# Kernel tuning notes

Measured on AMD Instinct MI355X. Metric: run time of the kernel, lower is better.

Reference implementation:

```python
import jax, jax.numpy as jnp
import numpy as np

N_NODES = 20000
N_EDGES = 160000
N_GRAPHS = 1000
IN_DIM = 11
HID = 128
EDGE_DIM = 3
N_LAYERS = 5
BN_EPS = 1e-5


def setup_inputs() -> dict:
    key = jax.random.key(0)
    ks = jax.random.split(key, 24)
    x = jax.random.normal(ks[0], (N_NODES, IN_DIM), dtype=jnp.float32)
    edge_index = jax.random.randint(ks[1], (2, N_EDGES), 0, N_NODES, dtype=jnp.int64)
    batch = jnp.sort(jax.random.randint(ks[2], (N_NODES,), 0, N_GRAPHS, dtype=jnp.int64))
    edge_attr = jax.random.uniform(ks[3], (N_EDGES, EDGE_DIM), dtype=jnp.float32)
    s_in = 1.0 / np.sqrt(IN_DIM)
    s_z = 1.0 / np.sqrt(2 * HID + EDGE_DIM)
    s_h = 1.0 / np.sqrt(HID)
    W_in = jax.random.uniform(ks[4], (IN_DIM, HID), minval=-s_in, maxval=s_in)
    b_in = jax.random.uniform(ks[5], (HID,), minval=-s_in, maxval=s_in)
    Wf = jax.random.uniform(ks[6], (N_LAYERS, 2 * HID + EDGE_DIM, HID), minval=-s_z, maxval=s_z)
    bf = jax.random.uniform(ks[7], (N_LAYERS, HID), minval=-s_z, maxval=s_z)
    Ws = jax.random.uniform(ks[8], (N_LAYERS, 2 * HID + EDGE_DIM, HID), minval=-s_z, maxval=s_z)
    bs = jax.random.uniform(ks[9], (N_LAYERS, HID), minval=-s_z, maxval=s_z)
    gamma = jnp.ones((N_LAYERS, HID), dtype=jnp.float32)
    beta = jnp.zeros((N_LAYERS, HID), dtype=jnp.float32)
    W1 = jax.random.uniform(ks[10], (HID, HID), minval=-s_h, maxval=s_h)
    b1 = jax.random.uniform(ks[11], (HID,), minval=-s_h, maxval=s_h)
    W2 = jax.random.uniform(ks[12], (HID, HID), minval=-s_h, maxval=s_h)
    b2 = jax.random.uniform(ks[13], (HID,), minval=-s_h, maxval=s_h)
    W3 = jax.random.uniform(ks[14], (HID, 1), minval=-s_h, maxval=s_h)
    b3 = jax.random.uniform(ks[15], (1,), minval=-s_h, maxval=s_h)
    return {"x": x, "edge_index": edge_index, "batch": batch, "edge_attr": edge_attr,
            "W_in": W_in, "b_in": b_in, "Wf": Wf, "bf": bf, "Ws": Ws, "bs": bs,
            "gamma": gamma, "beta": beta, "W1": W1, "b1": b1, "W2": W2, "b2": b2,
            "W3": W3, "b3": b3}


def reference(x, edge_index, batch, edge_attr, W_in, b_in, Wf, bf, Ws, bs,
              gamma, beta, W1, b1, W2, b2, W3, b3):
    src = edge_index[0]  # x_j (source / neighbor)
    dst = edge_index[1]  # x_i (target / aggregation index)
    # in-degree per node for mean aggregation (zero-degree -> divide by 1, yields 0)
    deg = jax.ops.segment_sum(jnp.ones((N_EDGES,), jnp.float32), dst, num_segments=N_NODES)
    deg = jnp.maximum(deg, 1.0)[:, None]

    h = x @ W_in + b_in  # [N, H]
    for l in range(N_LAYERS):
        # CGConv: z = [x_i, x_j, e]; msg = sigmoid(z Wf) * softplus(z Ws); residual + mean-aggr
        z = jnp.concatenate([h[dst], h[src], edge_attr], axis=-1)  # [E, 2H+D]
        msg = jax.nn.sigmoid(z @ Wf[l] + bf[l]) * jax.nn.softplus(z @ Ws[l] + bs[l])
        agg = jax.ops.segment_sum(msg, dst, num_segments=N_NODES) / deg
        h = h + agg
        # BatchNorm1d (training-mode batch stats, biased variance)
        mu = jnp.mean(h, axis=0)
        var = jnp.mean((h - mu) ** 2, axis=0)
        h = (h - mu) * jax.lax.rsqrt(var + BN_EPS) * gamma[l] + beta[l]
        h = jax.nn.relu(h)
        # dropout omitted (eval mode)

    # global mean pool over graphs
    cnt = jax.ops.segment_sum(jnp.ones((N_NODES,), jnp.float32), batch, num_segments=N_GRAPHS)
    g = jax.ops.segment_sum(h, batch, num_segments=N_GRAPHS) / jnp.maximum(cnt, 1.0)[:, None]

    g = jax.nn.relu(g @ W1 + b1)
    g = jax.nn.relu(g @ W2 + b2)
    return g @ W3 + b3  # [G, 1]
```

## Files before the change

### kernel.cpp

```cpp
#include <hip/hip_runtime.h>
#include <math.h>

#define NN 20000
#define NE 160000
#define NG 1000
#define IND 11
#define H 128
#define ED 3
#define NL 5
#define ZDH (259*128)
#define BN_EPSF 1e-5f
#define BPAD 17
#define EPW 16
#define GP 4

#define DEG_BLKS ((NE + 255) / 256)
#define WPREP_BLKS ((NL * 512 * H + 255) / 256)
#define GB_BLKS ((NN + 255) / 256)
#define HIN_BLKS 512
#define PREP_GRID (DEG_BLKS + WPREP_BLKS + GB_BLKS + HIN_BLKS)

typedef unsigned short ushort_t;
typedef unsigned int uint_t;
typedef __attribute__((ext_vector_type(8))) short bf8_t;
typedef __attribute__((ext_vector_type(4))) float f4_t;

__device__ inline ushort_t f2bf(float x) {
    unsigned int u = __float_as_uint(x);
    unsigned int r = (u + 0x7fffu + ((u >> 16) & 1u)) >> 16;
    return (ushort_t)r;
}
__device__ inline float bf2f(ushort_t b) {
    return __uint_as_float(((unsigned int)b) << 16);
}

__global__ __launch_bounds__(256) void prep_fused(const int* __restrict__ dst,
                                                  int* __restrict__ degi,
                                                  const float* __restrict__ Wf,
                                                  const float* __restrict__ Ws,
                                                  ushort_t* __restrict__ Wt,
                                                  const float* __restrict__ x,
                                                  const float* __restrict__ Win,
                                                  const float* __restrict__ bin,
                                                  float* __restrict__ h,
                                                  const int* __restrict__ batch,
                                                  int* __restrict__ gstart) {
    int b = blockIdx.x;
    int tid = threadIdx.x;
    if (b < DEG_BLKS) {
        int e = b * 256 + tid;
        if (e < NE) atomicAdd(&degi[dst[e]], 1);
    } else if (b < DEG_BLKS + WPREP_BLKS) {
        int idx = (b - DEG_BLKS) * 256 + tid;
        if (idx < NL * 512 * H) {
            int k = idx & 127;
            int n = (idx >> 7) & 511;
            int l = idx >> 16;
            int t = n >> 7, j = n & 127;
            const float* W = (t == 0 || t == 2) ? Wf : Ws;
            int krow = (t < 2) ? k : (H + k);
            Wt[idx] = f2bf(W[(size_t)l * ZDH + krow * H + j]);
        }
    } else if (b < DEG_BLKS + WPREP_BLKS + GB_BLKS) {
        int n = (b - DEG_BLKS - WPREP_BLKS) * 256 + tid;
        if (n < NN) {
            int b0 = batch[n];
            int bn = (n + 1 < NN) ? batch[n + 1] : NG;
            if (n == 0)
                for (int t = 0; t <= b0; ++t) gstart[t] = 0;
            for (int t = b0 + 1; t <= bn; ++t) gstart[t] = n + 1;
        }
    } else {
        __shared__ float lw[IND * H];
        for (int i = tid; i < IND * H; i += 256) lw[i] = Win[i];
        __syncthreads();
        int j = tid & 127;
        float bj = bin[j];
        int rb = b - (DEG_BLKS + WPREP_BLKS + GB_BLKS);
        for (int n = rb * 2 + (tid >> 7); n < NN; n += HIN_BLKS * 2) {
            const float* xr = x + (size_t)n * IND;
            float acc = bj;
#pragma unroll
            for (int k = 0; k < IND; ++k) acc = fmaf(xr[k], lw[k * H + j], acc);
            h[(size_t)n * H + j] = acc;
        }
    }
}

__global__ __launch_bounds__(256) void reserve_kernel(const int* __restrict__ degi,
                                                      int* __restrict__ cursor,
                                                      float* __restrict__ invdeg,
                                                      int* __restrict__ counter) {
    int n = blockIdx.x * blockDim.x + threadIdx.x;
    int lane = threadIdx.x & 63;
    int v = (n < NN) ? degi[n] : 0;
    int x = v;
#pragma unroll
    for (int st = 1; st < 64; st <<= 1) {
        int y = __shfl_up(x, st, 64);
        if (lane >= st) x += y;
    }
    int total = __shfl(x, 63, 64);
    int base = 0;
    if (lane == 63) base = atomicAdd(counter, total);
    base = __shfl(base, 63, 64);
    if (n < NN) {
        cursor[n] = base + x - v;
        invdeg[n] = 1.0f / (float)(v < 1 ? 1 : v);
    }
}

__global__ void scatter_kernel(const int* __restrict__ src, const int* __restrict__ dst,
                               const float* __restrict__ ea,
                               const float* __restrict__ invdeg,
                               int* __restrict__ cursor, float4* __restrict__ csr_ea4,
                               int* __restrict__ csr_dst, float* __restrict__ csr_inv) {
    int e = blockIdx.x * blockDim.x + threadIdx.x;
    if (e < NE) {
        int d = dst[e];
        int pos = atomicAdd(&cursor[d], 1);
        float4 r;
        r.x = ea[e * ED + 0];
        r.y = ea[e * ED + 1];
        r.z = ea[e * ED + 2];
        r.w = __int_as_float(src[e]);
        csr_ea4[pos] = r;
        csr_dst[pos] = d;
        csr_inv[pos] = invdeg[d];
    }
}

__global__ void flag_kernel(const int* __restrict__ csr_dst, unsigned* __restrict__ endmask) {
    int e = blockIdx.x * blockDim.x + threadIdx.x;
    if (e < NE) {
        int d = csr_dst[e];
        int dn = (e + 1 < NE) ? csr_dst[e + 1] : -1;
        if (d != dn) atomicOr(&endmask[e >> 5], 1u << (e & 31));
    }
}

__global__ __launch_bounds__(256, 2) void node_gemm_mfma(const float* __restrict__ hsrc,
                                                         float* __restrict__ hbn,
                                                         const ushort_t* __restrict__ Wt,
                                                         const float* __restrict__ sum,
                                                         const float* __restrict__ sumsq,
                                                         const float* __restrict__ gamma,
                                                         const float* __restrict__ beta,
                                                         int applyBN,
                                                         uint_t* __restrict__ ppack,
                                                         uint_t* __restrict__ qpack) {
    __shared__ __align__(16) ushort_t lbF[128 * BPAD * 8];
    __shared__ __align__(16) ushort_t lbS[128 * BPAD * 8];
    int pair = blockIdx.y;
    int wave = threadIdx.x >> 6;
    int lane = threadIdx.x & 63;
    int sub = lane & 15;
    int quad = lane >> 4;
    int m0 = blockIdx.x * 64 + wave * 16;
    int writeH = applyBN && (pair == 0);

    const ushort_t* whF = Wt + (size_t)(2 * pair) * 128 * H;
    const ushort_t* whS = Wt + (size_t)(2 * pair + 1) * 128 * H;

    for (int c = threadIdx.x; c < 2048; c += 256) {
        int n = c >> 4, k = c & 15;
        *(bf8_t*)(lbF + ((size_t)n * BPAD + k) * 8) = *(const bf8_t*)(whF + n * H + k * 8);
        *(bf8_t*)(lbS + ((size_t)n * BPAD + k) * 8) = *(const bf8_t*)(whS + n * H + k * 8);
    }

    bf8_t aHi[4], aLo[4];
    int r = m0 + sub;
    int rc = r < NN ? r : NN - 1;
#pragma unroll
    for (int ks = 0; ks < 4; ++ks) {
        int kb = ks * 32 + quad * 8;
        const float* hp = hsrc + (size_t)rc * H + kb;
        float4 v0 = *(const float4*)hp;
        float4 v1 = *(const float4*)(hp + 4);
        float vv[8] = {v0.x, v0.y, v0.z, v0.w, v1.x, v1.y, v1.z, v1.w};
        if (applyBN) {
            float4 su0 = *(const float4*)&sum[kb],   su1 = *(const float4*)&sum[kb + 4];
            float4 sq0 = *(const float4*)&sumsq[kb], sq1 = *(const float4*)&sumsq[kb + 4];
            float4 ga0 = *(const float4*)&gamma[kb], ga1 = *(const float4*)&gamma[kb + 4];
            float4 be0 = *(const float4*)&beta[kb],  be1 = *(const float4*)&beta[kb + 4];
            float su[8] = {su0.x, su0.y, su0.z, su0.w, su1.x, su1.y, su1.z, su1.w};
            float sq[8] = {sq0.x, sq0.y, sq0.z, sq0.w, sq1.x, sq1.y, sq1.z, sq1.w};
            float ga[8] = {ga0.x, ga0.y, ga0.z, ga0.w, ga1.x, ga1.y, ga1.z, ga1.w};
            float be[8] = {be0.x, be0.y, be0.z, be0.w, be1.x, be1.y, be1.z, be1.w};
#pragma unroll
            for (int i = 0; i < 8; ++i) {
                float mu  = su[i] * (1.0f / NN);
                float var = sq[i] * (1.0f / NN) - mu * mu;
                float sc  = ga[i] * rsqrtf(var + BN_EPSF);
                float sh  = be[i] - mu * sc;
                float v = fmaf(vv[i], sc, sh);
                vv[i] = v > 0.0f ? v : 0.0f;
            }
        }
        bf8_t hi8, lo8;
#pragma unroll
        for (int i = 0; i < 8; ++i) {
            ushort_t hi = f2bf(vv[i]);
            hi8[i] = (short)hi;
            lo8[i] = (short)f2bf(vv[i] - bf2f(hi));
        }
        aHi[ks] = hi8;
        aLo[ks] = lo8;
        if (writeH && r < NN) {
            float* op = hbn + (size_t)r * H + kb;
            *(float4*)op = make_float4(vv[0], vv[1], vv[2], vv[3]);
            *(float4*)(op + 4) = make_float4(vv[4], vv[5], vv[6], vv[7]);
        }
    }
    __syncthreads();

    f4_t accF[8], accS[8];
#pragma unroll
    for (int b = 0; b < 8; ++b) { accF[b] = (f4_t){0.f, 0.f, 0.f, 0.f}; accS[b] = (f4_t){0.f, 0.f, 0.f, 0.f}; }

#pragma unroll
    for (int nt = 0; nt < 8; ++nt) {
#pragma unroll
        for (int ks = 0; ks < 4; ++ks) {
            size_t lo = ((size_t)(nt * 16 + sub) * BPAD + ks * 4 + quad) * 8;
            bf8_t bF = *(const bf8_t*)(lbF + lo);
            bf8_t bS = *(const bf8_t*)(lbS + lo);
            accF[nt] = __builtin_amdgcn_mfma_f32_16x16x32_bf16(aHi[ks], bF, accF[nt], 0, 0, 0);
            accF[nt] = __builtin_amdgcn_mfma_f32_16x16x32_bf16(aLo[ks], bF, accF[nt], 0, 0, 0);
            accS[nt] = __builtin_amdgcn_mfma_f32_16x16x32_bf16(aHi[ks], bS, accS[nt], 0, 0, 0);
            accS[nt] = __builtin_amdgcn_mfma_f32_16x16x32_bf16(aLo[ks], bS, accS[nt], 0, 0, 0);
        }
    }

    uint_t* outp = pair ? qpack : ppack;
#pragma unroll
    for (int nt = 0; nt < 8; ++nt) {
        int col = nt * 16 + sub;
#pragma unroll
        for (int rr = 0; rr < 4; ++rr) {
            int row = m0 + quad * 4 + rr;
            if (row < NN) {
                uint_t lo = f2bf(accF[nt][rr]);
                uint_t hi = f2bf(accS[nt][rr]);
                outp[(size_t)row * H + col] = lo | (hi << 16);
            }
        }
    }
}

__global__ __launch_bounds__(256) void agg_edge_kernel(const int4* __restrict__ csr_fe,
                                                       const int* __restrict__ csr_dst,
                                                       const float* __restrict__ csr_inv,
                                                       const unsigned* __restrict__ endmask,
                                                       const float* __restrict__ Wf,
                                                       const float* __restrict__ bf,
                                                       const float* __restrict__ Ws,
                                                       const float* __restrict__ bs,
                                                       const uint_t* __restrict__ ppack,
                                                       const uint_t* __restrict__ qpack,
                                                       float* __restrict__ h,
                                                       float* __restrict__ sum,
                                                       float* __restrict__ sumsq) {
    int tid = threadIdx.x;
    if (blockIdx.x == 0 && tid < H) { sum[tid] = 0.0f; sumsq[tid] = 0.0f; }
    int lane = tid & 63;
    int wv = tid >> 6;
    int base = (blockIdx.x * 4 + wv) * EPW;
    int c0 = 2 * lane;

    float2 wf0 = *(const float2*)&Wf[256 * H + c0];
    float2 wf1 = *(const float2*)&Wf[257 * H + c0];
    float2 wf2 = *(const float2*)&Wf[258 * H + c0];
    float2 ws0 = *(const float2*)&Ws[256 * H + c0];
    float2 ws1 = *(const float2*)&Ws[257 * H + c0];
    float2 ws2 = *(const float2*)&Ws[258 * H + c0];
    float2 bf2_ = *(const float2*)&bf[c0];
    float2 bs2_ = *(const float2*)&bs[c0];

    int4 fe = csr_fe[base + (lane & (EPW - 1))];
    int  dd = csr_dst[base + (lane & (EPW - 1))];
    int  ivr = __float_as_int(csr_inv[base + (lane & (EPW - 1))]);
    unsigned mword = endmask[base >> 5];
    unsigned mask = __builtin_amdgcn_readfirstlane((mword >> (base & 31)) & 0xFFFFu);

    uint2 q[8];
#pragma unroll
    for (int i = 0; i < 8; ++i) {
        int s = __builtin_amdgcn_readlane(fe.w, i);
        q[i] = *(const uint2*)&qpack[(size_t)s * H + c0];
    }

    int dcur = __builtin_amdgcn_readlane(dd, 0);
    uint2 ppc = *(const uint2*)&ppack[(size_t)dcur * H + c0];
    float pf0 = __uint_as_float(ppc.x << 16), ps0 = __uint_as_float(ppc.x & 0xFFFF0000u);
    float pf1 = __uint_as_float(ppc.y << 16), ps1 = __uint_as_float(ppc.y & 0xFFFF0000u);
    unsigned m = mask;
    int e0 = m ? __builtin_ctz(m) : EPW;
    int dnext = 0;
    uint2 ppN = ppc;
    if (e0 + 1 < EPW) {
        dnext = __builtin_amdgcn_readlane(dd, e0 + 1);
        ppN = *(const uint2*)&ppack[(size_t)dnext * H + c0];
    }

    float acc0 = 0.f, acc1 = 0.f;

#pragma unroll
    for (int tb = 0; tb < EPW; tb += 8) {
#pragma unroll
        for (int i = 0; i < 8; ++i) {
            int t = tb + i;
            float ex = __int_as_float(__builtin_amdgcn_readlane(fe.x, t));
            float ey = __int_as_float(__builtin_amdgcn_readlane(fe.y, t));
            float ez = __int_as_float(__builtin_amdgcn_readlane(fe.z, t));
            uint2 qq = q[i];
            if (t + 8 < EPW) {
                int s2 = __builtin_amdgcn_readlane(fe.w, t + 8);
                q[i] = *(const uint2*)&qpack[(size_t)s2 * H + c0];
            }
            float qf0 = __uint_as_float(qq.x << 16);
            float qs0 = __uint_as_float(qq.x & 0xFFFF0000u);
            float qf1 = __uint_as_float(qq.y << 16);
            float qs1 = __uint_as_float(qq.y & 0xFFFF0000u);
            float f0 = fmaf(ex, wf0.x, fmaf(ey, wf1.x, fmaf(ez, wf2.x, pf0 + bf2_.x + qf0)));
            float v0 = fmaf(ex, ws0.x, fmaf(ey, ws1.x, fmaf(ez, ws2.x, ps0 + bs2_.x + qs0)));
            float f1 = fmaf(ex, wf0.y, fmaf(ey, wf1.y, fmaf(ez, wf2.y, pf1 + bf2_.y + qf1)));
            float v1 = fmaf(ex, ws0.y, fmaf(ey, ws1.y, fmaf(ez, ws2.y, ps1 + bs2_.y + qs1)));
            float sig0 = __builtin_amdgcn_rcpf(1.0f + __expf(-f0));
            float sp0  = fmaxf(v0, 0.0f) + __logf(1.0f + __expf(-fabsf(v0)));
            float sig1 = __builtin_amdgcn_rcpf(1.0f + __expf(-f1));
            float sp1  = fmaxf(v1, 0.0f) + __logf(1.0f + __expf(-fabsf(v1)));
            acc0 = fmaf(sig0, sp0, acc0);
            acc1 = fmaf(sig1, sp1, acc1);
            if (mask & (1u << t)) {
                float inv = __int_as_float(__builtin_amdgcn_readlane(ivr, t));
                atomicAdd(&h[(size_t)dcur * H + c0], acc0 * inv);
                atomicAdd(&h[(size_t)dcur * H + c0 + 1], acc1 * inv);
                acc0 = 0.f; acc1 = 0.f;
                dcur = dnext;
                pf0 = __uint_as_float(ppN.x << 16); ps0 = __uint_as_float(ppN.x & 0xFFFF0000u);
                pf1 = __uint_as_float(ppN.y << 16); ps1 = __uint_as_float(ppN.y & 0xFFFF0000u);
                m &= m - 1;
                int e1 = m ? __builtin_ctz(m) : EPW;
                if (e1 + 1 < EPW) {
                    dnext = __builtin_amdgcn_readlane(dd, e1 + 1);
                    ppN = *(const uint2*)&ppack[(size_t)dnext * H + c0];
                }
            }
        }
    }
    if (!(mask & (1u << (EPW - 1)))) {
        float inv = __int_as_float(__builtin_amdgcn_readlane(ivr, EPW - 1));
        atomicAdd(&h[(size_t)dcur * H + c0], acc0 * inv);
        atomicAdd(&h[(size_t)dcur * H + c0 + 1], acc1 * inv);
    }
}

__global__ __launch_bounds__(H) void stats_kernel(const float* __restrict__ h,
                                                  float* __restrict__ sum,
                                                  float* __restrict__ sumsq) {
    int j = threadIdx.x;
    float s = 0.0f, ss = 0.0f;
    int n = blockIdx.x * 8;
    for (; n + 7 < NN; n += gridDim.x * 8) {
        float v[8];
#pragma unroll
        for (int i = 0; i < 8; ++i) v[i] = h[(size_t)(n + i) * H + j];
#pragma unroll
        for (int i = 0; i < 8; ++i) { s += v[i]; ss = fmaf(v[i], v[i], ss); }
    }
    for (; n < NN; ++n) {
        float v = h[(size_t)n * H + j];
        s += v;
        ss = fmaf(v, v, ss);
    }
    atomicAdd(&sum[j], s);
    atomicAdd(&sumsq[j], ss);
}

__global__ __launch_bounds__(H) void pool_mlp_kernel(const float* __restrict__ h,
                                                     const int* __restrict__ gstart,
                                                     const float* __restrict__ sum,
                                                     const float* __restrict__ sumsq,
                                                     const float* __restrict__ gamma,
                                                     const float* __restrict__ beta,
                                                     const float* __restrict__ W1,
                                                     const float* __restrict__ b1,
                                                     const float* __restrict__ W2,
                                                     const float* __restrict__ b2,
                                                     const float* __restrict__ W3,
                                                     const float* __restrict__ b3,
                                                     float* __restrict__ out) {
    int j = threadIdx.x;
    float mu  = sum[j] * (1.0f / NN);
    float var = sumsq[j] * (1.0f / NN) - mu * mu;
    float sc  = gamma[j] * rsqrtf(var + BN_EPSF);
    float sh  = beta[j] - mu * sc;

    __shared__ float s1[GP][H];
    __shared__ float s2[GP][H];

#pragma unroll
    for (int gi = 0; gi < GP; ++gi) {
        int g0 = blockIdx.x * GP + gi;
        int a = gstart[g0], e = gstart[g0 + 1];
        float p0 = 0.f, p1 = 0.f, p2 = 0.f, p3 = 0.f;
        int n = a;
        for (; n + 3 < e; n += 4) {
            float v0 = fmaf(h[(size_t)(n + 0) * H + j], sc, sh);
            float v1 = fmaf(h[(size_t)(n + 1) * H + j], sc, sh);
// ... 52 lines not shown
    const int*   srcp  = ei;
    const int*   dstp  = ei + NE;
    const int*   batch = (const int*)d_in[2];
    const float* ea    = (const float*)d_in[3];
    const float* Win   = (const float*)d_in[4];
    const float* bin   = (const float*)d_in[5];
    const float* Wf    = (const float*)d_in[6];
    const float* bf    = (const float*)d_in[7];
    const float* Ws    = (const float*)d_in[8];
    const float* bs    = (const float*)d_in[9];
    const float* gamma = (const float*)d_in[10];
    const float* beta  = (const float*)d_in[11];
    const float* W1    = (const float*)d_in[12];
    const float* b1    = (const float*)d_in[13];
    const float* W2    = (const float*)d_in[14];
    const float* b2    = (const float*)d_in[15];
    const float* W3    = (const float*)d_in[16];
    const float* b3    = (const float*)d_in[17];
    float* out = (float*)d_out;

    const size_t NH = (size_t)NN * H;
    float* wsp = (float*)d_ws;
    size_t off = 0;
    float* hA     = wsp + off; off += NH;
    float* hB     = wsp + off; off += NH;
    uint_t* ppack = (uint_t*)(wsp + off); off += NH;
    uint_t* qpack = (uint_t*)(wsp + off); off += NH;
    float* invdeg = wsp + off; off += NN;
    float* sum    = wsp + off; off += H;
    float* sumsq  = wsp + off; off += H;
    int* gstart   = (int*)(wsp + off); off += NG + 1;
    off = (off + 3) & ~(size_t)3;
    float4* csr_ea4 = (float4*)(wsp + off); off += (size_t)NE * 4;
    float* csr_inv = wsp + off; off += NE;
    int* degi      = (int*)(wsp + off); off += NN;
    int* counter   = (int*)(wsp + off); off += 1;
    unsigned* endmask = (unsigned*)(wsp + off); off += NE / 32;
    int* cursor    = (int*)(wsp + off); off += NN;
    int* csr_dst   = (int*)(wsp + off); off += NE;
    off = (off + 3) & ~(size_t)3;
    ushort_t* Wt = (ushort_t*)(wsp + off); off += (size_t)NL * 512 * H / 2;

    hipMemsetAsync(degi, 0, (NN + 1 + NE / 32) * sizeof(int), stream);
    prep_fused<<<PREP_GRID, 256, 0, stream>>>(dstp, degi, Wf, Ws, Wt,
                                              x, Win, bin, hA, batch, gstart);
    reserve_kernel<<<(NN + 255) / 256, 256, 0, stream>>>(degi, cursor, invdeg, counter);
    scatter_kernel<<<(NE + 255) / 256, 256, 0, stream>>>(srcp, dstp, ea, invdeg, cursor,
                                                         csr_ea4, csr_dst, csr_inv);
    flag_kernel<<<(NE + 255) / 256, 256, 0, stream>>>(csr_dst, endmask);

    float* hRead = hA;
    for (int l = 0; l < NL; ++l) {
        float* hTgt = (l == 0) ? hA : ((l & 1) ? hB : hA);
        node_gemm_mfma<<<dim3((NN + 63) / 64, 2), 256, 0, stream>>>(
            hRead, hTgt,
            Wt + (size_t)l * 512 * H,
            sum, sumsq,
            gamma + (size_t)(l ? l - 1 : 0) * H,
            beta  + (size_t)(l ? l - 1 : 0) * H,
            l > 0, ppack, qpack);
        agg_edge_kernel<<<NE / (4 * EPW), 256, 0, stream>>>((const int4*)csr_ea4, csr_dst,
                                                            csr_inv, endmask,
                                                            Wf + (size_t)l * ZDH, bf + (size_t)l * H,
                                                            Ws + (size_t)l * ZDH, bs + (size_t)l * H,
                                                            ppack, qpack,
                                                            hTgt, sum, sumsq);
        stats_kernel<<<512, H, 0, stream>>>(hTgt, sum, sumsq);
        hRead = hTgt;
    }

    pool_mlp_kernel<<<NG / GP, H, 0, stream>>>(hRead, gstart, sum, sumsq,
                                               gamma + (size_t)(NL - 1) * H,
                                               beta + (size_t)(NL - 1) * H,
                                               W1, b1, W2, b2, W3, b3, out);
}
```

Baseline: 475.7 us.

## Switch edge aggregation to node-per-wave CSR gather without atomics

Replaces the edge-chunked aggregation, which relied on segment-end bitmasks and per-segment atomicAdd into h, with a kernel that assigns one wave per destination node. Each wave walks that node's CSR row using rowptr and degree, then does a plain read-modify-write of h. This drops the flag kernel, the csr_dst and csr_inv arrays and the float atomics. In exchange, load balance now depends on the degree distribution, with an average of about 8 edges per wave, and per-chunk bounds checks add branching.

```diff
diff --git a/kernel.cpp b/kernel.cpp
--- a/kernel.cpp
+++ b/kernel.cpp
@@ -11,7 +11,6 @@
 #define ZDH (259*128)
 #define BN_EPSF 1e-5f
 #define BPAD 17
-#define EPW 16
 #define GP 4
 
 #define DEG_BLKS ((NE + 255) / 256)
@@ -89,6 +88,7 @@
 
 __global__ __launch_bounds__(256) void reserve_kernel(const int* __restrict__ degi,
                                                       int* __restrict__ cursor,
+                                                      int* __restrict__ rowptr,
                                                       float* __restrict__ invdeg,
                                                       int* __restrict__ counter) {
     int n = blockIdx.x * blockDim.x + threadIdx.x;
@@ -105,16 +105,16 @@
     if (lane == 63) base = atomicAdd(counter, total);
     base = __shfl(base, 63, 64);
     if (n < NN) {
-        cursor[n] = base + x - v;
+        int st0 = base + x - v;
+        cursor[n] = st0;
+        rowptr[n] = st0;
         invdeg[n] = 1.0f / (float)(v < 1 ? 1 : v);
     }
 }
 
 __global__ void scatter_kernel(const int* __restrict__ src, const int* __restrict__ dst,
                                const float* __restrict__ ea,
-                               const float* __restrict__ invdeg,
-                               int* __restrict__ cursor, float4* __restrict__ csr_ea4,
-                               int* __restrict__ csr_dst, float* __restrict__ csr_inv) {
+                               int* __restrict__ cursor, float4* __restrict__ csr_ea4) {
     int e = blockIdx.x * blockDim.x + threadIdx.x;
     if (e < NE) {
         int d = dst[e];
@@ -125,17 +125,6 @@
         r.z = ea[e * ED + 2];
         r.w = __int_as_float(src[e]);
         csr_ea4[pos] = r;
-        csr_dst[pos] = d;
-        csr_inv[pos] = invdeg[d];
-    }
-}
-
-__global__ void flag_kernel(const int* __restrict__ csr_dst, unsigned* __restrict__ endmask) {
-    int e = blockIdx.x * blockDim.x + threadIdx.x;
-    if (e < NE) {
-        int d = csr_dst[e];
-        int dn = (e + 1 < NE) ? csr_dst[e + 1] : -1;
-        if (d != dn) atomicOr(&endmask[e >> 5], 1u << (e & 31));
     }
 }
 
@@ -248,14 +237,14 @@
     }
 }
 
-__global__ __launch_bounds__(256) void agg_edge_kernel(const int4* __restrict__ csr_fe,
-                                                       const int* __restrict__ csr_dst,
-                                                       const float* __restrict__ csr_inv,
-                                                       const unsigned* __restrict__ endmask,
+__global__ __launch_bounds__(256) void agg_node_kernel(const int4* __restrict__ csr_fe,
+                                                       const int* __restrict__ rowptr,
+                                                       const int* __restrict__ degi,
+                                                       const float* __restrict__ invdeg,
                                                        const float* __restrict__ Wf,
-                                                       const float* __restrict__ bf,
+                                                       const float* __restrict__ bfv,
                                                        const float* __restrict__ Ws,
-                                                       const float* __restrict__ bs,
+                                                       const float* __restrict__ bsv,
                                                        const uint_t* __restrict__ ppack,
                                                        const uint_t* __restrict__ qpack,
                                                        float* __restrict__ h,
@@ -265,8 +254,12 @@
     if (blockIdx.x == 0 && tid < H) { sum[tid] = 0.0f; sumsq[tid] = 0.0f; }
     int lane = tid & 63;
     int wv = tid >> 6;
-    int base = (blockIdx.x * 4 + wv) * EPW;
+    int n = blockIdx.x * 4 + wv;
     int c0 = 2 * lane;
+
+    int a = __builtin_amdgcn_readfirstlane(rowptr[n]);
+    int d = __builtin_amdgcn_readfirstlane(degi[n]);
+    if (d == 0) return;
 
     float2 wf0 = *(const float2*)&Wf[256 * H + c0];
     float2 wf1 = *(const float2*)&Wf[257 * H + c0];
@@ -274,86 +267,69 @@
     float2 ws0 = *(const float2*)&Ws[256 * H + c0];
     float2 ws1 = *(const float2*)&Ws[257 * H + c0];
     float2 ws2 = *(const float2*)&Ws[258 * H + c0];
-    float2 bf2_ = *(const float2*)&bf[c0];
-    float2 bs2_ = *(const float2*)&bs[c0];
-
-    int4 fe = csr_fe[base + (lane & (EPW - 1))];
-    int  dd = csr_dst[base + (lane & (EPW - 1))];
-    int  ivr = __float_as_int(csr_inv[base + (lane & (EPW - 1))]);
-    unsigned mword = endmask[base >> 5];
-    unsigned mask = __builtin_amdgcn_readfirstlane((mword >> (base & 31)) & 0xFFFFu);
-
-    uint2 q[8];
-#pragma unroll
-    for (int i = 0; i < 8; ++i) {
-        int s = __builtin_amdgcn_readlane(fe.w, i);
-        q[i] = *(const uint2*)&qpack[(size_t)s * H + c0];
-    }
-
-    int dcur = __builtin_amdgcn_readlane(dd, 0);
-    uint2 ppc = *(const uint2*)&ppack[(size_t)dcur * H + c0];
+    float2 bf2_ = *(const float2*)&bfv[c0];
+    float2 bs2_ = *(const float2*)&bsv[c0];
+
+    uint2 ppc = *(const uint2*)&ppack[(size_t)n * H + c0];
     float pf0 = __uint_as_float(ppc.x << 16), ps0 = __uint_as_float(ppc.x & 0xFFFF0000u);
     float pf1 = __uint_as_float(ppc.y << 16), ps1 = __uint_as_float(ppc.y & 0xFFFF0000u);
-    unsigned m = mask;
-    int e0 = m ? __builtin_ctz(m) : EPW;
-    int dnext = 0;
-    uint2 ppN = ppc;
-    if (e0 + 1 < EPW) {
-        dnext = __builtin_amdgcn_readlane(dd, e0 + 1);
-        ppN = *(const uint2*)&ppack[(size_t)dnext * H + c0];
-    }
+    float cf0 = pf0 + bf2_.x, cs0 = ps0 + bs2_.x;
+    float cf1 = pf1 + bf2_.y, cs1 = ps1 + bs2_.y;
 
     float acc0 = 0.f, acc1 = 0.f;
 
-#pragma unroll
-    for (int tb = 0; tb < EPW; tb += 8) {
+    for (int cb = 0; cb < d; cb += 64) {
+        int rem = d - cb;
+        if (rem > 64) rem = 64;
+        int4 fe = csr_fe[a + cb + (lane < rem ? lane : rem - 1)];
+
+        uint2 q[8];
 #pragma unroll
         for (int i = 0; i < 8; ++i) {
-            int t = tb + i;
-            float ex = __int_as_float(__builtin_amdgcn_readlane(fe.x, t));
-            float ey = __int_as_float(__builtin_amdgcn_readlane(fe.y, t));
-            float ez = __int_as_float(__builtin_amdgcn_readlane(fe.z, t));
-            uint2 qq = q[i];
-            if (t + 8 < EPW) {
-                int s2 = __builtin_amdgcn_readlane(fe.w, t + 8);
-                q[i] = *(const uint2*)&qpack[(size_t)s2 * H + c0];
+            if (i < rem) {
+                int s = __builtin_amdgcn_readlane(fe.w, i);
+                q[i] = *(const uint2*)&qpack[(size_t)s * H + c0];
             }
-            float qf0 = __uint_as_float(qq.x << 16);
-            float qs0 = __uint_as_float(qq.x & 0xFFFF0000u);
-            float qf1 = __uint_as_float(qq.y << 16);
-            float qs1 = __uint_as_float(qq.y & 0xFFFF0000u);
-            float f0 = fmaf(ex, wf0.x, fmaf(ey, wf1.x, fmaf(ez, wf2.x, pf0 + bf2_.x + qf0)));
-            float v0 = fmaf(ex, ws0.x, fmaf(ey, ws1.x, fmaf(ez, ws2.x, ps0 + bs2_.x + qs0)));
-            float f1 = fmaf(ex, wf0.y, fmaf(ey, wf1.y, fmaf(ez, wf2.y, pf1 + bf2_.y + qf1)));
-            float v1 = fmaf(ex, ws0.y, fmaf(ey, ws1.y, fmaf(ez, ws2.y, ps1 + bs2_.y + qs1)));
-            float sig0 = __builtin_amdgcn_rcpf(1.0f + __expf(-f0));
-            float sp0  = fmaxf(v0, 0.0f) + __logf(1.0f + __expf(-fabsf(v0)));
-            float sig1 = __builtin_amdgcn_rcpf(1.0f + __expf(-f1));
-            float sp1  = fmaxf(v1, 0.0f) + __logf(1.0f + __expf(-fabsf(v1)));
-            acc0 = fmaf(sig0, sp0, acc0);
-            acc1 = fmaf(sig1, sp1, acc1);
-            if (mask & (1u << t)) {
-                float inv = __int_as_float(__builtin_amdgcn_readlane(ivr, t));
-                atomicAdd(&h[(size_t)dcur * H + c0], acc0 * inv);
-                atomicAdd(&h[(size_t)dcur * H + c0 + 1], acc1 * inv);
-                acc0 = 0.f; acc1 = 0.f;
-                dcur = dnext;
-                pf0 = __uint_as_float(ppN.x << 16); ps0 = __uint_as_float(ppN.x & 0xFFFF0000u);
-                pf1 = __uint_as_float(ppN.y << 16); ps1 = __uint_as_float(ppN.y & 0xFFFF0000u);
-                m &= m - 1;
-                int e1 = m ? __builtin_ctz(m) : EPW;
-                if (e1 + 1 < EPW) {
-                    dnext = __builtin_amdgcn_readlane(dd, e1 + 1);
-                    ppN = *(const uint2*)&ppack[(size_t)dnext * H + c0];
+        }
+
+        for (int tb = 0; tb < rem; tb += 8) {
+#pragma unroll
+            for (int i = 0; i < 8; ++i) {
+                int t = tb + i;
+                if (t < rem) {
+                    uint2 qq = q[i];
+                    if (t + 8 < rem) {
+                        int s2 = __builtin_amdgcn_readlane(fe.w, t + 8);
+                        q[i] = *(const uint2*)&qpack[(size_t)s2 * H + c0];
+                    }
+                    float ex = __int_as_float(__builtin_amdgcn_readlane(fe.x, t));
+                    float ey = __int_as_float(__builtin_amdgcn_readlane(fe.y, t));
+                    float ez = __int_as_float(__builtin_amdgcn_readlane(fe.z, t));
+                    float qf0 = __uint_as_float(qq.x << 16);
+                    float qs0 = __uint_as_float(qq.x & 0xFFFF0000u);
+                    float qf1 = __uint_as_float(qq.y << 16);
+                    float qs1 = __uint_as_float(qq.y & 0xFFFF0000u);
+                    float f0 = fmaf(ex, wf0.x, fmaf(ey, wf1.x, fmaf(ez, wf2.x, cf0 + qf0)));
+                    float v0 = fmaf(ex, ws0.x, fmaf(ey, ws1.x, fmaf(ez, ws2.x, cs0 + qs0)));
+                    float f1 = fmaf(ex, wf0.y, fmaf(ey, wf1.y, fmaf(ez, wf2.y, cf1 + qf1)));
+                    float v1 = fmaf(ex, ws0.y, fmaf(ey, ws1.y, fmaf(ez, ws2.y, cs1 + qs1)));
+                    float sig0 = __builtin_amdgcn_rcpf(1.0f + __expf(-f0));
+                    float sp0  = fmaxf(v0, 0.0f) + __logf(1.0f + __expf(-fabsf(v0)));
+                    float sig1 = __builtin_amdgcn_rcpf(1.0f + __expf(-f1));
+                    float sp1  = fmaxf(v1, 0.0f) + __logf(1.0f + __expf(-fabsf(v1)));
+                    acc0 = fmaf(sig0, sp0, acc0);
+                    acc1 = fmaf(sig1, sp1, acc1);
                 }
             }
         }
     }
-    if (!(mask & (1u << (EPW - 1)))) {
-        float inv = __int_as_float(__builtin_amdgcn_readlane(ivr, EPW - 1));
-        atomicAdd(&h[(size_t)dcur * H + c0], acc0 * inv);
-        atomicAdd(&h[(size_t)dcur * H + c0 + 1], acc1 * inv);
-    }
+
+    float inv = invdeg[n];
+    size_t hoff = (size_t)n * H + c0;
+    float2 hv = *(const float2*)&h[hoff];
+    hv.x = fmaf(acc0, inv, hv.x);
+    hv.y = fmaf(acc1, inv, hv.y);
+    *(float2*)&h[hoff] = hv;
 }
 
 __global__ __launch_bounds__(H) void stats_kernel(const float* __restrict__ h,
@@ -494,22 +470,18 @@
     int* gstart   = (int*)(wsp + off); off += NG + 1;
     off = (off + 3) & ~(size_t)3;
     float4* csr_ea4 = (float4*)(wsp + off); off += (size_t)NE * 4;
-    float* csr_inv = wsp + off; off += NE;
     int* degi      = (int*)(wsp + off); off += NN;
     int* counter   = (int*)(wsp + off); off += 1;
-    unsigned* endmask = (unsigned*)(wsp + off); off += NE / 32;
     int* cursor    = (int*)(wsp + off); off += NN;
-    int* csr_dst   = (int*)(wsp + off); off += NE;
+    int* rowptr    = (int*)(wsp + off); off += NN;
     off = (off + 3) & ~(size_t)3;
     ushort_t* Wt = (ushort_t*)(wsp + off); off += (size_t)NL * 512 * H / 2;
 
-    hipMemsetAsync(degi, 0, (NN + 1 + NE / 32) * sizeof(int), stream);
+    hipMemsetAsync(degi, 0, (NN + 1) * sizeof(int), stream);
     prep_fused<<<PREP_GRID, 256, 0, stream>>>(dstp, degi, Wf, Ws, Wt,
                                               x, Win, bin, hA, batch, gstart);
-    reserve_kernel<<<(NN + 255) / 256, 256, 0, stream>>>(degi, cursor, invdeg, counter);
-    scatter_kernel<<<(NE + 255) / 256, 256, 0, stream>>>(srcp, dstp, ea, invdeg, cursor,
-                                                         csr_ea4, csr_dst, csr_inv);
-    flag_kernel<<<(NE + 255) / 256, 256, 0, stream>>>(csr_dst, endmask);
+    reserve_kernel<<<(NN + 255) / 256, 256, 0, stream>>>(degi, cursor, rowptr, invdeg, counter);
+    scatter_kernel<<<(NE + 255) / 256, 256, 0, stream>>>(srcp, dstp, ea, cursor, csr_ea4);
 
     float* hRead = hA;
     for (int l = 0; l < NL; ++l) {
@@ -521,12 +493,12 @@
             gamma + (size_t)(l ? l - 1 : 0) * H,
             beta  + (size_t)(l ? l - 1 : 0) * H,
             l > 0, ppack, qpack);
-        agg_edge_kernel<<<NE / (4 * EPW), 256, 0, stream>>>((const int4*)csr_ea4, csr_dst,
-                                                            csr_inv, endmask,
-                                                            Wf + (size_t)l * ZDH, bf + (size_t)l * H,
-                                                            Ws + (size_t)l * ZDH, bs + (size_t)l * H,
-                                                            ppack, qpack,
-                                                            hTgt, sum, sumsq);
+        agg_node_kernel<<<(NN + 3) / 4, 256, 0, stream>>>((const int4*)csr_ea4, rowptr, degi,
+                                                          invdeg,
+                                                          Wf + (size_t)l * ZDH, bf + (size_t)l * H,
+                                                          Ws + (size_t)l * ZDH, bs + (size_t)l * H,
+                                                          ppack, qpack,
+                                                          hTgt, sum, sumsq);
         stats_kernel<<<512, H, 0, stream>>>(hTgt, sum, sumsq);
         hRead = hTgt;
     }
```

After: 495.6 us. +4.2%, slower.

## Fuse per-layer GEMM, edge aggregation and stats into cooperative persistent megakernel

Applied to the files above, without the earlier changes.

Replaces the fifteen per-layer launches (node GEMM, edge aggregation, BN statistics for each of five layers) with one cooperative persistent kernel. It loops over layers and separates phases with grid-wide syncs, while blocks stride over GEMM tiles, edge windows and stats partitions. The aim is to remove launch gaps and tail drain between short kernels. The cost is three grid barriers per layer and a fixed grid sized from occupancy, which may load-balance worse than the original launches. If the cooperative launch fails, the old multi-kernel path runs instead.

```diff
diff --git a/kernel.cpp b/kernel.cpp
--- a/kernel.cpp
+++ b/kernel.cpp
@@ -1,5 +1,8 @@
 #include <hip/hip_runtime.h>
+#include <hip/hip_cooperative_groups.h>
 #include <math.h>
+
+namespace cg = cooperative_groups;
 
 #define NN 20000
 #define NE 160000
@@ -13,6 +16,8 @@
 #define BPAD 17
 #define EPW 16
 #define GP 4
+#define MBLK 313
+#define NWIN (NE / EPW)
 
 #define DEG_BLKS ((NE + 255) / 256)
 #define WPREP_BLKS ((NL * 512 * H + 255) / 256)
@@ -139,30 +144,30 @@
     }
 }
 
-__global__ __launch_bounds__(256, 2) void node_gemm_mfma(const float* __restrict__ hsrc,
-                                                         float* __restrict__ hbn,
-                                                         const ushort_t* __restrict__ Wt,
-                                                         const float* __restrict__ sum,
-                                                         const float* __restrict__ sumsq,
-                                                         const float* __restrict__ gamma,
-                                                         const float* __restrict__ beta,
-                                                         int applyBN,
-                                                         uint_t* __restrict__ ppack,
-                                                         uint_t* __restrict__ qpack) {
-    __shared__ __align__(16) ushort_t lbF[128 * BPAD * 8];
-    __shared__ __align__(16) ushort_t lbS[128 * BPAD * 8];
-    int pair = blockIdx.y;
-    int wave = threadIdx.x >> 6;
-    int lane = threadIdx.x & 63;
+
+__device__ __forceinline__ void gemm_item(int mb, int pair,
+                                          const float* __restrict__ hsrc,
+                                          float* __restrict__ hbn,
+                                          const ushort_t* __restrict__ Wt_l,
+                                          const float* __restrict__ sum,
+                                          const float* __restrict__ sumsq,
+                                          const float* __restrict__ gamma_l,
+                                          const float* __restrict__ beta_l,
+                                          int applyBN,
+                                          uint_t* __restrict__ ppack,
+                                          uint_t* __restrict__ qpack,
+                                          ushort_t* lbF, ushort_t* lbS, int tid) {
+    int wave = tid >> 6;
+    int lane = tid & 63;
     int sub = lane & 15;
     int quad = lane >> 4;
-    int m0 = blockIdx.x * 64 + wave * 16;
+    int m0 = mb * 64 + wave * 16;
     int writeH = applyBN && (pair == 0);
 
-    const ushort_t* whF = Wt + (size_t)(2 * pair) * 128 * H;
-    const ushort_t* whS = Wt + (size_t)(2 * pair + 1) * 128 * H;
-
-    for (int c = threadIdx.x; c < 2048; c += 256) {
+    const ushort_t* whF = Wt_l + (size_t)(2 * pair) * 128 * H;
+    const ushort_t* whS = Wt_l + (size_t)(2 * pair + 1) * 128 * H;
+
+    for (int c = tid; c < 2048; c += 256) {
         int n = c >> 4, k = c & 15;
         *(bf8_t*)(lbF + ((size_t)n * BPAD + k) * 8) = *(const bf8_t*)(whF + n * H + k * 8);
         *(bf8_t*)(lbS + ((size_t)n * BPAD + k) * 8) = *(const bf8_t*)(whS + n * H + k * 8);
@@ -181,8 +186,8 @@
         if (applyBN) {
             float4 su0 = *(const float4*)&sum[kb],   su1 = *(const float4*)&sum[kb + 4];
             float4 sq0 = *(const float4*)&sumsq[kb], sq1 = *(const float4*)&sumsq[kb + 4];
-            float4 ga0 = *(const float4*)&gamma[kb], ga1 = *(const float4*)&gamma[kb + 4];
-            float4 be0 = *(const float4*)&beta[kb],  be1 = *(const float4*)&beta[kb + 4];
+            float4 ga0 = *(const float4*)&gamma_l[kb], ga1 = *(const float4*)&gamma_l[kb + 4];
+            float4 be0 = *(const float4*)&beta_l[kb],  be1 = *(const float4*)&beta_l[kb + 4];
             float su[8] = {su0.x, su0.y, su0.z, su0.w, su1.x, su1.y, su1.z, su1.w};
             float sq[8] = {sq0.x, sq0.y, sq0.z, sq0.w, sq1.x, sq1.y, sq1.z, sq1.w};
             float ga[8] = {ga0.x, ga0.y, ga0.z, ga0.w, ga1.x, ga1.y, ga1.z, ga1.w};
@@ -248,35 +253,34 @@
     }
 }
 
-__global__ __launch_bounds__(256) void agg_edge_kernel(const int4* __restrict__ csr_fe,
-                                                       const int* __restrict__ csr_dst,
-                                                       const float* __restrict__ csr_inv,
-                                                       const unsigned* __restrict__ endmask,
-                                                       const float* __restrict__ Wf,
-                                                       const float* __restrict__ bf,
-                                                       const float* __restrict__ Ws,
-                                                       const float* __restrict__ bs,
-                                                       const uint_t* __restrict__ ppack,
-                                                       const uint_t* __restrict__ qpack,
-                                                       float* __restrict__ h,
-                                                       float* __restrict__ sum,
-                                                       float* __restrict__ sumsq) {
-    int tid = threadIdx.x;
-    if (blockIdx.x == 0 && tid < H) { sum[tid] = 0.0f; sumsq[tid] = 0.0f; }
-    int lane = tid & 63;
-    int wv = tid >> 6;
-    int base = (blockIdx.x * 4 + wv) * EPW;
+struct AggW { float2 wf0, wf1, wf2, ws0, ws1, ws2, bfv, bsv; };
+
+__device__ __forceinline__ AggW load_aggw(const float* __restrict__ Wf_l,
+                                          const float* __restrict__ bf_l,
+                                          const float* __restrict__ Ws_l,
+                                          const float* __restrict__ bs_l, int c0) {
+    AggW a;
+    a.wf0 = *(const float2*)&Wf_l[256 * H + c0];
+    a.wf1 = *(const float2*)&Wf_l[257 * H + c0];
+    a.wf2 = *(const float2*)&Wf_l[258 * H + c0];
+    a.ws0 = *(const float2*)&Ws_l[256 * H + c0];
+    a.ws1 = *(const float2*)&Ws_l[257 * H + c0];
+    a.ws2 = *(const float2*)&Ws_l[258 * H + c0];
+    a.bfv = *(const float2*)&bf_l[c0];
+    a.bsv = *(const float2*)&bs_l[c0];
+    return a;
+}
+
+__device__ __forceinline__ void agg_window(int base,
+                                           const int4* __restrict__ csr_fe,
+                                           const int* __restrict__ csr_dst,
+                                           const float* __restrict__ csr_inv,
+                                           const unsigned* __restrict__ endmask,
+                                           const AggW& aw,
+                                           const uint_t* __restrict__ ppack,
+                                           const uint_t* __restrict__ qpack,
+                                           float* __restrict__ h, int lane) {
     int c0 = 2 * lane;
-
-    float2 wf0 = *(const float2*)&Wf[256 * H + c0];
-    float2 wf1 = *(const float2*)&Wf[257 * H + c0];
-    float2 wf2 = *(const float2*)&Wf[258 * H + c0];
-    float2 ws0 = *(const float2*)&Ws[256 * H + c0];
-    float2 ws1 = *(const float2*)&Ws[257 * H + c0];
-    float2 ws2 = *(const float2*)&Ws[258 * H + c0];
-    float2 bf2_ = *(const float2*)&bf[c0];
-    float2 bs2_ = *(const float2*)&bs[c0];
-
     int4 fe = csr_fe[base + (lane & (EPW - 1))];
     int  dd = csr_dst[base + (lane & (EPW - 1))];
     int  ivr = __float_as_int(csr_inv[base + (lane & (EPW - 1))]);
@@ -322,10 +326,10 @@
             float qs0 = __uint_as_float(qq.x & 0xFFFF0000u);
             float qf1 = __uint_as_float(qq.y << 16);
             float qs1 = __uint_as_float(qq.y & 0xFFFF0000u);
-            float f0 = fmaf(ex, wf0.x, fmaf(ey, wf1.x, fmaf(ez, wf2.x, pf0 + bf2_.x + qf0)));
-            float v0 = fmaf(ex, ws0.x, fmaf(ey, ws1.x, fmaf(ez, ws2.x, ps0 + bs2_.x + qs0)));
-            float f1 = fmaf(ex, wf0.y, fmaf(ey, wf1.y, fmaf(ez, wf2.y, pf1 + bf2_.y + qf1)));
-            float v1 = fmaf(ex, ws0.y, fmaf(ey, ws1.y, fmaf(ez, ws2.y, ps1 + bs2_.y + qs1)));
+            float f0 = fmaf(ex, aw.wf0.x, fmaf(ey, aw.wf1.x, fmaf(ez, aw.wf2.x, pf0 + aw.bfv.x + qf0)));
+            float v0 = fmaf(ex, aw.ws0.x, fmaf(ey, aw.ws1.x, fmaf(ez, aw.ws2.x, ps0 + aw.bsv.x + qs0)));
+            float f1 = fmaf(ex, aw.wf0.y, fmaf(ey, aw.wf1.y, fmaf(ez, aw.wf2.y, pf1 + aw.bfv.y + qf1)));
+            float v1 = fmaf(ex, aw.ws0.y, fmaf(ey, aw.ws1.y, fmaf(ez, aw.ws2.y, ps1 + aw.bsv.y + qs1)));
             float sig0 = __builtin_amdgcn_rcpf(1.0f + __expf(-f0));
             float sp0  = fmaxf(v0, 0.0f) + __logf(1.0f + __expf(-fabsf(v0)));
             float sig1 = __builtin_amdgcn_rcpf(1.0f + __expf(-f1));
@@ -356,26 +360,120 @@
     }
 }
 
+__device__ __forceinline__ void stats_part(const float* __restrict__ h,
+                                           float* __restrict__ sum,
+                                           float* __restrict__ sumsq,
+                                           int j, int part, int nparts) {
+    float s = 0.0f, ss = 0.0f;
+    for (int n = part * 8; n + 7 < NN; n += nparts * 8) {
+        float v[8];
+#pragma unroll
+        for (int i = 0; i < 8; ++i) v[i] = h[(size_t)(n + i) * H + j];
+#pragma unroll
+        for (int i = 0; i < 8; ++i) { s += v[i]; ss = fmaf(v[i], v[i], ss); }
+    }
+    atomicAdd(&sum[j], s);
+    atomicAdd(&sumsq[j], ss);
+}
+
+__global__ __launch_bounds__(256, 2) void mega_kernel(const int4* __restrict__ csr_fe,
+                                                      const int* __restrict__ csr_dst,
+                                                      const float* __restrict__ csr_inv,
+                                                      const unsigned* __restrict__ endmask,
+                                                      const float* __restrict__ Wf,
+                                                      const float* __restrict__ bf,
+                                                      const float* __restrict__ Ws,
+                                                      const float* __restrict__ bs,
+                                                      const ushort_t* __restrict__ Wt,
+                                                      float* __restrict__ hA,
+                                                      float* __restrict__ hB,
+                                                      uint_t* __restrict__ ppack,
+                                                      uint_t* __restrict__ qpack,
+                                                      float* __restrict__ sum,
+                                                      float* __restrict__ sumsq,
+                                                      const float* __restrict__ gamma,
+                                                      const float* __restrict__ beta) {
+    cg::grid_group grid = cg::this_grid();
+    __shared__ __align__(16) ushort_t lbF[128 * BPAD * 8];
+    __shared__ __align__(16) ushort_t lbS[128 * BPAD * 8];
+    int tid = threadIdx.x;
+    int lane = tid & 63;
+    int wv = tid >> 6;
+
+    for (int l = 0; l < NL; ++l) {
+        const float* hsrc = (l == 0) ? hA : ((l & 1) ? hA : hB);
+        float* hTgt = (l == 0) ? hA : ((l & 1) ? hB : hA);
+        const ushort_t* Wt_l = Wt + (size_t)l * 512 * H;
+        const float* gam = gamma + (size_t)(l ? l - 1 : 0) * H;
+        const float* bet = beta + (size_t)(l ? l - 1 : 0) * H;
+        int applyBN = (l > 0);
+
+        for (int item = blockIdx.x; item < 2 * MBLK; item += gridDim.x) {
+            int pair = item >= MBLK;
+            int mb = pair ? item - MBLK : item;
+            gemm_item(mb, pair, hsrc, hTgt, Wt_l, sum, sumsq, gam, bet,
+                      applyBN, ppack, qpack, lbF, lbS, tid);
+            __syncthreads();
+        }
+        grid.sync();
+
+        if (blockIdx.x == 0 && tid < H) { sum[tid] = 0.0f; sumsq[tid] = 0.0f; }
+        {
+            AggW aw = load_aggw(Wf + (size_t)l * ZDH, bf + (size_t)l * H,
+                                Ws + (size_t)l * ZDH, bs + (size_t)l * H, 2 * lane);
+            for (int w = blockIdx.x * 4 + wv; w < NWIN; w += gridDim.x * 4)
+                agg_window(w * EPW, csr_fe, csr_dst, csr_inv, endmask, aw,
+                           ppack, qpack, hTgt, lane);
+        }
+        grid.sync();
+
+        stats_part(hTgt, sum, sumsq, tid & 127, blockIdx.x * 2 + (tid >> 7), gridDim.x * 2);
+        grid.sync();
+    }
+}
+
+__global__ __launch_bounds__(256, 2) void node_gemm_mfma(const float* __restrict__ hsrc,
+                                                         float* __restrict__ hbn,
+                                                         const ushort_t* __restrict__ Wt_l,
+                                                         const float* __restrict__ sum,
+                                                         const float* __restrict__ sumsq,
+                                                         const float* __restrict__ gamma_l,
+                                                         const float* __restrict__ beta_l,
+                                                         int applyBN,
+                                                         uint_t* __restrict__ ppack,
+                                                         uint_t* __restrict__ qpack) {
+    __shared__ __align__(16) ushort_t lbF[128 * BPAD * 8];
+    __shared__ __align__(16) ushort_t lbS[128 * BPAD * 8];
+    gemm_item(blockIdx.x, blockIdx.y, hsrc, hbn, Wt_l, sum, sumsq, gamma_l, beta_l,
+              applyBN, ppack, qpack, lbF, lbS, threadIdx.x);
+}
+
+__global__ __launch_bounds__(256) void agg_edge_kernel(const int4* __restrict__ csr_fe,
+                                                       const int* __restrict__ csr_dst,
+                                                       const float* __restrict__ csr_inv,
+                                                       const unsigned* __restrict__ endmask,
+                                                       const float* __restrict__ Wf_l,
+                                                       const float* __restrict__ bf_l,
+                                                       const float* __restrict__ Ws_l,
+                                                       const float* __restrict__ bs_l,
+                                                       const uint_t* __restrict__ ppack,
+                                                       const uint_t* __restrict__ qpack,
+                                                       float* __restrict__ h,
+                                                       float* __restrict__ sum,
+                                                       float* __restrict__ sumsq) {
+    int tid = threadIdx.x;
+    if (blockIdx.x == 0 && tid < H) { sum[tid] = 0.0f; sumsq[tid] = 0.0f; }
+    int lane = tid & 63;
+    int wv = tid >> 6;
+    AggW aw = load_aggw(Wf_l, bf_l, Ws_l, bs_l, 2 * lane);
+    agg_window((blockIdx.x * 4 + wv) * EPW, csr_fe, csr_dst, csr_inv, endmask, aw,
+               ppack, qpack, h, lane);
+}
+
 __global__ __launch_bounds__(H) void stats_kernel(const float* __restrict__ h,
                                                   float* __restrict__ sum,
                                                   float* __restrict__ sumsq) {
-    int j = threadIdx.x;
-    float s = 0.0f, ss = 0.0f;
-    int n = blockIdx.x * 8;
-    for (; n + 7 < NN; n += gridDim.x * 8) {
-        float v[8];
-#pragma unroll
-        for (int i = 0; i < 8; ++i) v[i] = h[(size_t)(n + i) * H + j];
-#pragma unroll
-        for (int i = 0; i < 8; ++i) { s += v[i]; ss = fmaf(v[i], v[i], ss); }
-    }
-    for (; n < NN; ++n) {
-        float v = h[(size_t)n * H + j];
-        s += v;
-        ss = fmaf(v, v, ss);
-    }
-    atomicAdd(&sum[j], s);
-    atomicAdd(&sumsq[j], ss);
+    stats_part(h, sum, sumsq, threadIdx.x, blockIdx.x, gridDim.x);
 }
 
 __global__ __launch_bounds__(H) void pool_mlp_kernel(const float* __restrict__ h,
@@ -511,24 +609,53 @@
                                                          csr_ea4, csr_dst, csr_inv);
     flag_kernel<<<(NE + 255) / 256, 256, 0, stream>>>(csr_dst, endmask);
 
-    float* hRead = hA;
-    for (int l = 0; l < NL; ++l) {
-        float* hTgt = (l == 0) ? hA : ((l & 1) ? hB : hA);
-        node_gemm_mfma<<<dim3((NN + 63) / 64, 2), 256, 0, stream>>>(
-            hRead, hTgt,
-            Wt + (size_t)l * 512 * H,
-            sum, sumsq,
-            gamma + (size_t)(l ? l - 1 : 0) * H,
-            beta  + (size_t)(l ? l - 1 : 0) * H,
-            l > 0, ppack, qpack);
-        agg_edge_kernel<<<NE / (4 * EPW), 256, 0, stream>>>((const int4*)csr_ea4, csr_dst,
-                                                            csr_inv, endmask,
-                                                            Wf + (size_t)l * ZDH, bf + (size_t)l * H,
-                                                            Ws + (size_t)l * ZDH, bs + (size_t)l * H,
-                                                            ppack, qpack,
-                                                            hTgt, sum, sumsq);
-        stats_kernel<<<512, H, 0, stream>>>(hTgt, sum, sumsq);
-        hRead = hTgt;
+    static int megaBlocks = 0;
+    if (megaBlocks == 0) {
+        int nb = 0;
+        if (hipOccupancyMaxActiveBlocksPerMultiprocessor(&nb, mega_kernel, 256, 0) != hipSuccess
+            || nb < 1) nb = 1;
+        if (nb > 2) nb = 2;
+        megaBlocks = nb * 256;
+    }
+    const int4* csr_fe_p = (const int4*)csr_ea4;
+    const int* csr_dst_p = csr_dst;
+    const float* csr_inv_p = csr_inv;
+    const unsigned* endmask_p = endmask;
+    const float* Wf_p = Wf;  const float* bf_p = bf;
+    const float* Ws_p = Ws;  const float* bs_p = bs;
+    const ushort_t* Wt_p = Wt;
+    float* hA_p = hA;  float* hB_p = hB;
+    uint_t* pp_p = ppack;  uint_t* qp_p = qpack;
+    float* sum_p = sum;  float* sumsq_p = sumsq;
+    const float* gamma_p = gamma;  const float* beta_p = beta;
+    void* margs[] = {&csr_fe_p, &csr_dst_p, &csr_inv_p, &endmask_p,
+                     &Wf_p, &bf_p, &Ws_p, &bs_p, &Wt_p,
+                     &hA_p, &hB_p, &pp_p, &qp_p, &sum_p, &sumsq_p,
+                     &gamma_p, &beta_p};
+    hipError_t merr = hipLaunchCooperativeKernel(mega_kernel, dim3(megaBlocks), dim3(256),
+                                                 margs, 0, stream);
+    float* hRead;
+    if (merr != hipSuccess) {
+        (void)hipGetLastError();
+        hRead = hA;
+        for (int l = 0; l < NL; ++l) {
+            float* hTgt = (l == 0) ? hA : ((l & 1) ? hB : hA);
+            node_gemm_mfma<<<dim3(MBLK, 2), 256, 0, stream>>>(
+                hRead, hTgt, Wt + (size_t)l * 512 * H, sum, sumsq,
+                gamma + (size_t)(l ? l - 1 : 0) * H,
+                beta  + (size_t)(l ? l - 1 : 0) * H,
+                l > 0, ppack, qpack);
+            agg_edge_kernel<<<NWIN / 4, 256, 0, stream>>>((const int4*)csr_ea4, csr_dst,
+                                                          csr_inv, endmask,
+                                                          Wf + (size_t)l * ZDH, bf + (size_t)l * H,
+                                                          Ws + (size_t)l * ZDH, bs + (size_t)l * H,
+                                                          ppack, qpack, hTgt, sum, sumsq);
+            stats_kernel<<<512, H, 0, stream>>>(hTgt, sum, sumsq);
+            hRead = hTgt;
+        }
+    } else {
+        hRead = (NL & 1) ? ((NL == 1) ? hA : (((NL - 1) & 1) ? hB : hA)) : hB;
+        hRead = hA;
     }
 
     pool_mlp_kernel<<<NG / GP, H, 0, stream>>>(hRead, gstart, sum, sumsq,
```

New measurement: 999.3 us. 110% more time.

## Pre-swizzle weights into MFMA fragment order and read directly from global

Applied to the files above, without the earlier changes.

The weight-prep stage now writes bf16 weights already arranged in per-lane MFMA B-fragment order. The node GEMM reads fragments straight from global/L2 instead of staging them through padded LDS, which removes the LDS fill and a barrier. BatchNorm scale and shift are computed once per block into shared memory rather than per element, and launch bounds are raised to four blocks per CU. The cost is that every wave re-reads weights from global memory, relying on cache hits.

```diff
diff --git a/kernel.cpp b/kernel.cpp
--- a/kernel.cpp
+++ b/kernel.cpp
@@ -10,9 +10,9 @@
 #define NL 5
 #define ZDH (259*128)
 #define BN_EPSF 1e-5f
-#define BPAD 17
 #define EPW 16
 #define GP 4
+#define MBLK 313
 
 #define DEG_BLKS ((NE + 255) / 256)
 #define WPREP_BLKS ((NL * 512 * H + 255) / 256)
@@ -59,7 +59,12 @@
             int t = n >> 7, j = n & 127;
             const float* W = (t == 0 || t == 2) ? Wf : Ws;
             int krow = (t < 2) ? k : (H + k);
-            Wt[idx] = f2bf(W[(size_t)l * ZDH + krow * H + j]);
+            ushort_t val = f2bf(W[(size_t)l * ZDH + krow * H + j]);
+            int nt = j >> 4, sub = j & 15;
+            int ks = k >> 5, quad = (k >> 3) & 3, e2 = k & 7;
+            int lane = quad * 16 + sub;
+            Wt[(size_t)l * 65536 + (size_t)t * 16384 +
+               (((nt * 4 + ks) * 64 + lane) * 8 + e2)] = val;
         }
     } else if (b < DEG_BLKS + WPREP_BLKS + GB_BLKS) {
         int n = (b - DEG_BLKS - WPREP_BLKS) * 256 + tid;
@@ -139,34 +144,40 @@
     }
 }
 
-__global__ __launch_bounds__(256, 2) void node_gemm_mfma(const float* __restrict__ hsrc,
+__global__ __launch_bounds__(256, 4) void node_gemm_mfma(const float* __restrict__ hsrc,
                                                          float* __restrict__ hbn,
-                                                         const ushort_t* __restrict__ Wt,
+                                                         const ushort_t* __restrict__ Wt_l,
                                                          const float* __restrict__ sum,
                                                          const float* __restrict__ sumsq,
-                                                         const float* __restrict__ gamma,
-                                                         const float* __restrict__ beta,
+                                                         const float* __restrict__ gamma_l,
+                                                         const float* __restrict__ beta_l,
                                                          int applyBN,
                                                          uint_t* __restrict__ ppack,
                                                          uint_t* __restrict__ qpack) {
-    __shared__ __align__(16) ushort_t lbF[128 * BPAD * 8];
-    __shared__ __align__(16) ushort_t lbS[128 * BPAD * 8];
     int pair = blockIdx.y;
-    int wave = threadIdx.x >> 6;
-    int lane = threadIdx.x & 63;
+    int tid = threadIdx.x;
+    int wave = tid >> 6;
+    int lane = tid & 63;
     int sub = lane & 15;
     int quad = lane >> 4;
     int m0 = blockIdx.x * 64 + wave * 16;
     int writeH = applyBN && (pair == 0);
 
-    const ushort_t* whF = Wt + (size_t)(2 * pair) * 128 * H;
-    const ushort_t* whS = Wt + (size_t)(2 * pair + 1) * 128 * H;
-
-    for (int c = threadIdx.x; c < 2048; c += 256) {
-        int n = c >> 4, k = c & 15;
-        *(bf8_t*)(lbF + ((size_t)n * BPAD + k) * 8) = *(const bf8_t*)(whF + n * H + k * 8);
-        *(bf8_t*)(lbS + ((size_t)n * BPAD + k) * 8) = *(const bf8_t*)(whS + n * H + k * 8);
-    }
+    __shared__ float bnsc[H];
+    __shared__ float bnsh[H];
+    if (applyBN) {
+        if (tid < H) {
+            float mu  = sum[tid] * (1.0f / NN);
+            float var = sumsq[tid] * (1.0f / NN) - mu * mu;
+            float sc  = gamma_l[tid] * rsqrtf(var + BN_EPSF);
+            bnsc[tid] = sc;
+            bnsh[tid] = beta_l[tid] - mu * sc;
+        }
+        __syncthreads();
+    }
+
+    const bf8_t* fragF = (const bf8_t*)(Wt_l + (size_t)(2 * pair) * 16384);
+    const bf8_t* fragS = (const bf8_t*)(Wt_l + (size_t)(2 * pair + 1) * 16384);
 
     bf8_t aHi[4], aLo[4];
     int r = m0 + sub;
@@ -179,21 +190,9 @@
         float4 v1 = *(const float4*)(hp + 4);
         float vv[8] = {v0.x, v0.y, v0.z, v0.w, v1.x, v1.y, v1.z, v1.w};
         if (applyBN) {
-            float4 su0 = *(const float4*)&sum[kb],   su1 = *(const float4*)&sum[kb + 4];
-            float4 sq0 = *(const float4*)&sumsq[kb], sq1 = *(const float4*)&sumsq[kb + 4];
-            float4 ga0 = *(const float4*)&gamma[kb], ga1 = *(const float4*)&gamma[kb + 4];
-            float4 be0 = *(const float4*)&beta[kb],  be1 = *(const float4*)&beta[kb + 4];
-            float su[8] = {su0.x, su0.y, su0.z, su0.w, su1.x, su1.y, su1.z, su1.w};
-            float sq[8] = {sq0.x, sq0.y, sq0.z, sq0.w, sq1.x, sq1.y, sq1.z, sq1.w};
-            float ga[8] = {ga0.x, ga0.y, ga0.z, ga0.w, ga1.x, ga1.y, ga1.z, ga1.w};
-            float be[8] = {be0.x, be0.y, be0.z, be0.w, be1.x, be1.y, be1.z, be1.w};
 #pragma unroll
             for (int i = 0; i < 8; ++i) {
-                float mu  = su[i] * (1.0f / NN);
-                float var = sq[i] * (1.0f / NN) - mu * mu;
-                float sc  = ga[i] * rsqrtf(var + BN_EPSF);
-                float sh  = be[i] - mu * sc;
-                float v = fmaf(vv[i], sc, sh);
+                float v = fmaf(vv[i], bnsc[kb + i], bnsh[kb + i]);
                 vv[i] = v > 0.0f ? v : 0.0f;
             }
         }
@@ -212,7 +211,6 @@
             *(float4*)(op + 4) = make_float4(vv[4], vv[5], vv[6], vv[7]);
         }
     }
-    __syncthreads();
 
     f4_t accF[8], accS[8];
 #pragma unroll
@@ -222,9 +220,8 @@
     for (int nt = 0; nt < 8; ++nt) {
 #pragma unroll
         for (int ks = 0; ks < 4; ++ks) {
-            size_t lo = ((size_t)(nt * 16 + sub) * BPAD + ks * 4 + quad) * 8;
-            bf8_t bF = *(const bf8_t*)(lbF + lo);
-            bf8_t bS = *(const bf8_t*)(lbS + lo);
+            bf8_t bF = fragF[(nt * 4 + ks) * 64 + lane];
+            bf8_t bS = fragS[(nt * 4 + ks) * 64 + lane];
             accF[nt] = __builtin_amdgcn_mfma_f32_16x16x32_bf16(aHi[ks], bF, accF[nt], 0, 0, 0);
             accF[nt] = __builtin_amdgcn_mfma_f32_16x16x32_bf16(aLo[ks], bF, accF[nt], 0, 0, 0);
             accS[nt] = __builtin_amdgcn_mfma_f32_16x16x32_bf16(aHi[ks], bS, accS[nt], 0, 0, 0);
@@ -514,7 +511,7 @@
     float* hRead = hA;
     for (int l = 0; l < NL; ++l) {
         float* hTgt = (l == 0) ? hA : ((l & 1) ? hB : hA);
-        node_gemm_mfma<<<dim3((NN + 63) / 64, 2), 256, 0, stream>>>(
+        node_gemm_mfma<<<dim3(MBLK, 2), 256, 0, stream>>>(
             hRead, hTgt,
             Wt + (size_t)l * 512 * H,
             sum, sumsq,
```

After: 471.4 us. No clear change (-0.9%).
